# Optimization experiments

Measured on AMD Instinct MI355X. Metric: run time of the kernel, lower is better.

The kernel has to match this reference:

```python
import jax, jax.numpy as jnp
import numpy as np

N, DIM, TOPK = 8192, 512, 10


def setup_inputs() -> dict:
    key = jax.random.key(0)
    k1, k2, k3, k4, k5 = jax.random.split(key, 5)
    s = DIM ** -0.5
    return {
        "X": jax.random.normal(k1, (N, DIM), dtype=jnp.float32),
        "Wh": jax.random.normal(k2, (DIM, DIM), dtype=jnp.float32) * s,
        "bh": jax.random.normal(k3, (DIM,), dtype=jnp.float32) * s,
        "Wt": jax.random.normal(k4, (DIM, DIM), dtype=jnp.float32) * s,
        "bt": jax.random.normal(k5, (DIM,), dtype=jnp.float32) * s,
    }


def reference(X, Wh, bh, Wt, bt):
    n, dim = X.shape
    scale = dim ** -0.5
    e_h = X @ Wh.T + bh                      # [n, dim]
    e_t = X @ Wt.T + bt                      # [n, dim]
    logits = (e_h @ e_t.T) * scale           # [n, n]
    topk_val, topk_idx = jax.lax.top_k(logits, TOPK)   # [n, k]
    weights = jax.nn.softmax(topk_val, axis=-1)        # [n, k]
    src = jnp.repeat(jnp.arange(n, dtype=jnp.int32), TOPK)  # [n*k]
    dst = topk_idx.reshape(-1).astype(jnp.int32)
    edge_index = jnp.stack([src, dst], axis=0)          # [2, n*k]
    edge_weight = weights.reshape(-1)                   # [n*k]
    return edge_index, edge_weight
```

## Files before the change

### kernel.cpp

```cpp
#include <hip/hip_runtime.h>
#include <math.h>

#define NROWS 8192
#define DIMK  512
#define TOPK  10
#define SCALE 0.044194173824159223f

#define ETM 128
#define ETN 64
#define ETK 32
#define NTHREADS 256

#define BM 128
#define BN 128
#define BK 32
#define NS2 16
#define SCOLS2 (NROWS / NS2)
#define NQ 256
#define CAP 64
#define TMARGIN 2.0f

typedef __attribute__((ext_vector_type(8))) short bf16x8;
typedef __attribute__((ext_vector_type(4))) float f32x4;

__device__ __forceinline__ unsigned short f2bf(float f) {
  unsigned int u = __float_as_uint(f);
  u = (u + 0x7FFF + ((u >> 16) & 1)) >> 16;
  return (unsigned short)u;
}

__device__ __forceinline__ void gld16(const void* g, const void* lds) {
  __builtin_amdgcn_global_load_lds(
      (const __attribute__((address_space(1))) void*)g,
      (__attribute__((address_space(3))) void*)lds, 16, 0, 0);
}

__global__ __launch_bounds__(NTHREADS, 4)
void embed_gemm(const float* __restrict__ X,
                const float* __restrict__ Wh, const float* __restrict__ bh,
                const float* __restrict__ Wt, const float* __restrict__ bt,
                float* __restrict__ Eh, float* __restrict__ Et,
                unsigned short* __restrict__ Ehb, unsigned short* __restrict__ Etb) {
  __shared__ float As[ETK][ETM + 4];
  __shared__ float Bs[ETK][ETN + 4];

  const int tid = threadIdx.x;
  const int rowBase = blockIdx.x * ETM;
  const int colBase = blockIdx.y * ETN;
  const float* W  = (colBase < DIMK) ? Wh : Wt;
  const float* bb = (colBase < DIMK) ? bh : bt;
  float* Out            = (colBase < DIMK) ? Eh : Et;
  unsigned short* Outb  = (colBase < DIMK) ? Ehb : Etb;
  const int colOff = colBase & (DIMK - 1);

  const int tx = tid & 15, ty = tid >> 4;
  float acc[8][4];
#pragma unroll
  for (int r = 0; r < 8; ++r)
#pragma unroll
    for (int c = 0; c < 4; ++c) acc[r][c] = 0.f;

  for (int kt = 0; kt < DIMK; kt += ETK) {
    __syncthreads();
#pragma unroll
    for (int u = 0; u < 4; ++u) {
      const int idx = tid + u * NTHREADS;
      const int r = idx >> 3;
      const int dc = idx & 7;
      const float4 av = *(const float4*)&X[(size_t)(rowBase + r) * DIMK + kt + dc * 4];
      As[dc * 4 + 0][r] = av.x; As[dc * 4 + 1][r] = av.y;
      As[dc * 4 + 2][r] = av.z; As[dc * 4 + 3][r] = av.w;
    }
#pragma unroll
    for (int u = 0; u < 2; ++u) {
      const int idx = tid + u * NTHREADS;
      const int r = idx >> 3;
      const int dc = idx & 7;
      const float4 bv = *(const float4*)&W[(size_t)(colOff + r) * DIMK + kt + dc * 4];
      Bs[dc * 4 + 0][r] = bv.x; Bs[dc * 4 + 1][r] = bv.y;
      Bs[dc * 4 + 2][r] = bv.z; Bs[dc * 4 + 3][r] = bv.w;
    }
    __syncthreads();
#pragma unroll 8
    for (int k = 0; k < ETK; ++k) {
      const float4 a0 = *(const float4*)&As[k][ty * 4];
      const float4 a1 = *(const float4*)&As[k][64 + ty * 4];
      const float4 b  = *(const float4*)&Bs[k][tx * 4];
      const float ar[8] = {a0.x, a0.y, a0.z, a0.w, a1.x, a1.y, a1.z, a1.w};
      const float br[4] = {b.x, b.y, b.z, b.w};
#pragma unroll
      for (int r = 0; r < 8; ++r)
#pragma unroll
        for (int c = 0; c < 4; ++c)
          acc[r][c] = fmaf(ar[r], br[c], acc[r][c]);
    }
  }

  const float4 bv = *(const float4*)&bb[colOff + tx * 4];
  const float br[4] = {bv.x, bv.y, bv.z, bv.w};
#pragma unroll
  for (int r = 0; r < 8; ++r) {
    const int row = rowBase + ((r < 4) ? (ty * 4 + r) : (64 + ty * 4 + r - 4));
    float4 o;
    o.x = acc[r][0] + br[0]; o.y = acc[r][1] + br[1];
    o.z = acc[r][2] + br[2]; o.w = acc[r][3] + br[3];
    const size_t off = (size_t)row * DIMK + colOff + tx * 4;
    *(float4*)&Out[off] = o;
    ushort4 ob;
    ob.x = f2bf(o.x); ob.y = f2bf(o.y); ob.z = f2bf(o.z); ob.w = f2bf(o.w);
    *(ushort4*)&Outb[off] = ob;
  }
}

__global__ __launch_bounds__(256, 3)
void screen_store(const unsigned short* __restrict__ Ehb,
                  const unsigned short* __restrict__ Etb,
                  float* __restrict__ tmax, unsigned short* __restrict__ Sc) {
  __shared__ unsigned short As[2][BM * BK];
  __shared__ unsigned short Bs[2][BN * BK];
  __shared__ unsigned short Csb[BM * 72];

  const int tid = threadIdx.x;
  const int rowBase = blockIdx.x * BM;
  const int strip = blockIdx.y;
  const int w = tid >> 6, lane = tid & 63;
  const int q = lane >> 4, l15 = lane & 15;
  const int wr = (w & 1) * 64, wc = (w >> 1) * 64;
  const int rr = tid >> 1, hq = tid & 1;

  const int c0 = tid, c1 = tid + 256;
  const int wb0 = __builtin_amdgcn_readfirstlane(tid & ~63);
  const int wb1 = wb0 + 256;
  const int ar0 = c0 >> 2, ac0 = (c0 & 3) * 8;
  const int ar1 = c1 >> 2, ac1 = (c1 & 3) * 8;

  for (int ct = 0; ct < SCOLS2; ct += BN) {
    const int colBase = strip * SCOLS2 + ct;
    const int tileG = colBase >> 7;
    f32x4 acc[4][4];
#pragma unroll
    for (int i = 0; i < 4; ++i)
#pragma unroll
      for (int j = 0; j < 4; ++j) acc[i][j] = (f32x4){0.f, 0.f, 0.f, 0.f};

    auto stage = [&](int buf, int kt) {
      gld16(Ehb + (size_t)(rowBase + ar0) * DIMK + kt + ac0, As[buf] + wb0 * 8);
      gld16(Ehb + (size_t)(rowBase + ar1) * DIMK + kt + ac1, As[buf] + wb1 * 8);
      gld16(Etb + (size_t)(colBase + ar0) * DIMK + kt + ac0, Bs[buf] + wb0 * 8);
      gld16(Etb + (size_t)(colBase + ar1) * DIMK + kt + ac1, Bs[buf] + wb1 * 8);
    };
    auto compute = [&](int buf) {
      bf16x8 af[4], bf[4];
#pragma unroll
      for (int i = 0; i < 4; ++i)
        af[i] = *(const bf16x8*)&As[buf][(wr + i * 16 + l15) * BK + q * 8];
#pragma unroll
      for (int j = 0; j < 4; ++j)
        bf[j] = *(const bf16x8*)&Bs[buf][(wc + j * 16 + l15) * BK + q * 8];
#pragma unroll
      for (int i = 0; i < 4; ++i)
#pragma unroll
        for (int j = 0; j < 4; ++j)
          acc[i][j] = __builtin_amdgcn_mfma_f32_16x16x32_bf16(af[i], bf[j], acc[i][j], 0, 0, 0);
    };

    stage(0, 0);
    __syncthreads();
#pragma unroll 1
    for (int ki = 0; ki < DIMK / BK; ki += 2) {
      if (ki + 1 < DIMK / BK) stage(1, (ki + 1) * BK);
      compute(0);
      __syncthreads();
      if (ki + 2 < DIMK / BK) stage(0, (ki + 2) * BK);
      compute(1);
      __syncthreads();
    }

#pragma unroll
    for (int half = 0; half < 2; ++half) {
      if ((w >> 1) == half) {
#pragma unroll
        for (int i = 0; i < 4; ++i)
#pragma unroll
          for (int j = 0; j < 4; ++j)
#pragma unroll
            for (int rg = 0; rg < 4; ++rg)
              Csb[(wr + i * 16 + q * 4 + rg) * 72 + j * 16 + l15] = f2bf(acc[i][j][rg]);
      }
      __syncthreads();
      float m = -INFINITY;
      uint4 buf4[4];
#pragma unroll
      for (int k = 0; k < 4; ++k) {
        buf4[k] = *(const uint4*)&Csb[rr * 72 + hq * 32 + k * 8];
        const unsigned int uu[4] = {buf4[k].x, buf4[k].y, buf4[k].z, buf4[k].w};
#pragma unroll
        for (int e = 0; e < 4; ++e) {
          m = fmaxf(m, __uint_as_float(uu[e] << 16));
          m = fmaxf(m, __uint_as_float(uu[e] & 0xFFFF0000u));
        }
      }
      tmax[(size_t)(rowBase + rr) * NQ + tileG * 4 + half * 2 + hq] = m;
      uint4* dst = (uint4*)&Sc[(size_t)(rowBase + rr) * NROWS + colBase + half * 64 + hq * 32];
#pragma unroll
      for (int k = 0; k < 4; ++k) dst[k] = buf4[k];
      __syncthreads();
    }
  }
}

__global__ __launch_bounds__(256)
void collect_scan(const unsigned short* __restrict__ Sc,
                  const float* __restrict__ tmax,
                  int* __restrict__ cnt, int* __restrict__ cand) {
  __shared__ int lcnt[4];
  const int lane = threadIdx.x & 63;
  const int wid = threadIdx.x >> 6;
  const int r = blockIdx.x * 4 + wid;

  if (threadIdx.x < 4) lcnt[threadIdx.x] = 0;
  __syncthreads();

  const f32x4 gm = *(const f32x4*)&tmax[(size_t)r * NQ + lane * 4];
  float a0 = gm[0], a1 = gm[1], a2 = gm[2], a3 = gm[3];
  float g = -INFINITY;
#pragma unroll 1
  for (int j = 0; j < TOPK; ++j) {
    const float lm = fmaxf(fmaxf(a0, a1), fmaxf(a2, a3));
    g = lm;
#pragma unroll
    for (int off = 32; off > 0; off >>= 1) g = fmaxf(g, __shfl_xor(g, off, 64));
    const unsigned long long ball = __ballot(lm == g);
    const int src = __ffsll((long long)ball) - 1;
    if (lane == src) {
      if      (a0 == g) a0 = -INFINITY;
      else if (a1 == g) a1 = -INFINITY;
      else if (a2 == g) a2 = -INFINITY;
      else              a3 = -INFINITY;
    }
  }
  const float tt = g - TMARGIN;

  const unsigned short* row = Sc + (size_t)r * NROWS;
#pragma unroll 1
  for (int it = 0; it < NROWS / 512; ++it) {
    const int c0 = it * 512 + lane * 8;
    const uint4 u = *(const uint4*)&row[c0];
    const unsigned int uu[4] = {u.x, u.y, u.z, u.w};
#pragma unroll
    for (int e = 0; e < 4; ++e) {
      const float lo = __uint_as_float(uu[e] << 16);
      const float hi = __uint_as_float(uu[e] & 0xFFFF0000u);
      if (lo >= tt) {
        const int p = atomicAdd(&lcnt[wid], 1);
        if (p < CAP) cand[(size_t)r * CAP + p] = c0 + 2 * e;
      }
      if (hi >= tt) {
        const int p = atomicAdd(&lcnt[wid], 1);
        if (p < CAP) cand[(size_t)r * CAP + p] = c0 + 2 * e + 1;
      }
    }
  }
  __syncthreads();
  if (threadIdx.x < 4) cnt[blockIdx.x * 4 + threadIdx.x] = min(lcnt[threadIdx.x], CAP);
}

__global__ __launch_bounds__(256)
void rescore_topk(const float* __restrict__ Eh, const float* __restrict__ Et,
                  const int* __restrict__ cnt, const int* __restrict__ cand,
                  float* __restrict__ out) {
  const int lane = threadIdx.x & 63;
  const int r = blockIdx.x * 4 + (threadIdx.x >> 6);
  const int n = cnt[r];
  const bool active = lane < n;
  const int col = active ? cand[(size_t)r * CAP + lane] : 0;

  const float* a = Eh + (size_t)r * DIMK;
  const float* b = Et + (size_t)col * DIMK;
  float p = 0.f;
#pragma unroll 4
  for (int k = 0; k < DIMK; k += 4) {
    const float4 av = *(const float4*)&a[k];
    const float4 bv = *(const float4*)&b[k];
    p = fmaf(av.x, bv.x, p);
    p = fmaf(av.y, bv.y, p);
    p = fmaf(av.z, bv.z, p);
    p = fmaf(av.w, bv.w, p);
  }
  float v = active ? p * SCALE : -INFINITY;
  const int vc = active ? col : 0x7FFFFFFF;

  float myv = -INFINITY; int myc = 0; float m = 0.f;
  float vv = v; int cc2 = vc;
#pragma unroll 1
  for (int j = 0; j < TOPK; ++j) {
    float bvv = vv; int bcc = cc2;
#pragma unroll
    for (int off = 32; off > 0; off >>= 1) {
      const float ov = __shfl_xor(bvv, off, 64);
      const int oc = __shfl_xor(bcc, off, 64);
      if (ov > bvv || (ov == bvv && oc < bcc)) { bvv = ov; bcc = oc; }
    }
    if (j == 0) m = bvv;
    if (lane == j) { myv = bvv; myc = bcc; }
    if (vv == bvv && cc2 == bcc) vv = -INFINITY;
  }

  float sum = 0.f;
#pragma unroll
  for (int j = 0; j < TOPK; ++j) sum += expf(__shfl(myv, j, 64) - m);
  const float inv = 1.0f / sum;

  if (lane < TOPK) {
    const size_t ro = (size_t)r * TOPK + lane;
    out[ro] = (float)r;
    out[(size_t)NROWS * TOPK + ro] = (float)myc;
    out[2 * (size_t)NROWS * TOPK + ro] = expf(myv - m) * inv;
  }
}

extern "C" void kernel_launch(void* const* d_in, const int* in_sizes, int n_in,
                              void* d_out, int out_size, void* d_ws, size_t ws_size,
                              hipStream_t stream) {
  const float* X  = (const float*)d_in[0];
  const float* Wh = (const float*)d_in[1];
  const float* bh = (const float*)d_in[2];
  const float* Wt = (const float*)d_in[3];
  const float* bt = (const float*)d_in[4];
  float* out = (float*)d_out;

  char* ws = (char*)d_ws;
  const size_t embB  = (size_t)NROWS * DIMK * sizeof(float);
  const size_t embBH = (size_t)NROWS * DIMK * sizeof(unsigned short);
  const size_t tmaxB = (size_t)NROWS * NQ * sizeof(float);
  const size_t cntB  = (size_t)NROWS * sizeof(int);
  const size_t candB = (size_t)NROWS * CAP * sizeof(int);
  float* Eh   = (float*)ws;
  float* Et   = (float*)(ws + embB);
  unsigned short* Ehb = (unsigned short*)(ws + 2 * embB);
  unsigned short* Etb = (unsigned short*)(ws + 2 * embB + embBH);
  float* tmax = (float*)(ws + 2 * embB + 2 * embBH);
  int*   cnt  = (int*)(ws + 2 * embB + 2 * embBH + tmaxB);
  int*   cand = (int*)(ws + 2 * embB + 2 * embBH + tmaxB + cntB);
  unsigned short* Sc = (unsigned short*)
      (ws + 2 * embB + 2 * embBH + tmaxB + cntB + candB);

  dim3 blk(NTHREADS);
  dim3 g1(NROWS / ETM, (2 * DIMK) / ETN);
  embed_gemm<<<g1, blk, 0, stream>>>(X, Wh, bh, Wt, bt, Eh, Et, Ehb, Etb);

  dim3 g2(NROWS / BM, NS2);
  screen_store<<<g2, blk, 0, stream>>>(Ehb, Etb, tmax, Sc);

  collect_scan<<<NROWS / 4, blk, 0, stream>>>(Sc, tmax, cnt, cand);

  rescore_topk<<<NROWS / 4, blk, 0, stream>>>(Eh, Et, cnt, cand, out);
}
```

Measured before the change: 429.4 us.

## Double-buffer embed GEMM LDS tiles and fuse candidate scan with rescore

The embedding GEMM now stages K-tiles into two LDS buffers so the next tile's global loads overlap the current tile's FMAs. This halves the barriers per tile but raises LDS use, and the occupancy hint drops to 3. The collect and rescore kernels are merged, so candidates stay in shared memory instead of round-tripping through global cnt/cand arrays, which also removes one kernel launch. The fused kernel holds more state per block, which may affect occupancy.

```diff
diff --git a/kernel.cpp b/kernel.cpp
--- a/kernel.cpp
+++ b/kernel.cpp
@@ -35,14 +35,14 @@
       (__attribute__((address_space(3))) void*)lds, 16, 0, 0);
 }
 
-__global__ __launch_bounds__(NTHREADS, 4)
+__global__ __launch_bounds__(NTHREADS, 3)
 void embed_gemm(const float* __restrict__ X,
                 const float* __restrict__ Wh, const float* __restrict__ bh,
                 const float* __restrict__ Wt, const float* __restrict__ bt,
                 float* __restrict__ Eh, float* __restrict__ Et,
                 unsigned short* __restrict__ Ehb, unsigned short* __restrict__ Etb) {
-  __shared__ float As[ETK][ETM + 4];
-  __shared__ float Bs[ETK][ETN + 4];
+  __shared__ float As[2][ETK][ETM + 4];
+  __shared__ float Bs[2][ETK][ETN + 4];
 
   const int tid = threadIdx.x;
   const int rowBase = blockIdx.x * ETM;
@@ -60,16 +60,15 @@
 #pragma unroll
     for (int c = 0; c < 4; ++c) acc[r][c] = 0.f;
 
-  for (int kt = 0; kt < DIMK; kt += ETK) {
-    __syncthreads();
+  auto stage = [&](int buf, int kt) {
 #pragma unroll
     for (int u = 0; u < 4; ++u) {
       const int idx = tid + u * NTHREADS;
       const int r = idx >> 3;
       const int dc = idx & 7;
       const float4 av = *(const float4*)&X[(size_t)(rowBase + r) * DIMK + kt + dc * 4];
-      As[dc * 4 + 0][r] = av.x; As[dc * 4 + 1][r] = av.y;
-      As[dc * 4 + 2][r] = av.z; As[dc * 4 + 3][r] = av.w;
+      As[buf][dc * 4 + 0][r] = av.x; As[buf][dc * 4 + 1][r] = av.y;
+      As[buf][dc * 4 + 2][r] = av.z; As[buf][dc * 4 + 3][r] = av.w;
     }
 #pragma unroll
     for (int u = 0; u < 2; ++u) {
@@ -77,15 +76,16 @@
       const int r = idx >> 3;
       const int dc = idx & 7;
       const float4 bv = *(const float4*)&W[(size_t)(colOff + r) * DIMK + kt + dc * 4];
-      Bs[dc * 4 + 0][r] = bv.x; Bs[dc * 4 + 1][r] = bv.y;
-      Bs[dc * 4 + 2][r] = bv.z; Bs[dc * 4 + 3][r] = bv.w;
-    }
-    __syncthreads();
-#pragma unroll 8
+      Bs[buf][dc * 4 + 0][r] = bv.x; Bs[buf][dc * 4 + 1][r] = bv.y;
+      Bs[buf][dc * 4 + 2][r] = bv.z; Bs[buf][dc * 4 + 3][r] = bv.w;
+    }
+  };
+  auto compute = [&](int buf) {
+#pragma unroll 4
     for (int k = 0; k < ETK; ++k) {
-      const float4 a0 = *(const float4*)&As[k][ty * 4];
-      const float4 a1 = *(const float4*)&As[k][64 + ty * 4];
-      const float4 b  = *(const float4*)&Bs[k][tx * 4];
+      const float4 a0 = *(const float4*)&As[buf][k][ty * 4];
+      const float4 a1 = *(const float4*)&As[buf][k][64 + ty * 4];
+      const float4 b  = *(const float4*)&Bs[buf][k][tx * 4];
       const float ar[8] = {a0.x, a0.y, a0.z, a0.w, a1.x, a1.y, a1.z, a1.w};
       const float br[4] = {b.x, b.y, b.z, b.w};
 #pragma unroll
@@ -94,6 +94,18 @@
         for (int c = 0; c < 4; ++c)
           acc[r][c] = fmaf(ar[r], br[c], acc[r][c]);
     }
+  };
+
+  stage(0, 0);
+  __syncthreads();
+#pragma unroll 1
+  for (int ki = 0; ki < DIMK / ETK; ki += 2) {
+    if (ki + 1 < DIMK / ETK) stage(1, (ki + 1) * ETK);
+    compute(0);
+    __syncthreads();
+    if (ki + 2 < DIMK / ETK) stage(0, (ki + 2) * ETK);
+    compute(1);
+    __syncthreads();
   }
 
   const float4 bv = *(const float4*)&bb[colOff + tx * 4];
@@ -210,15 +222,17 @@
 }
 
 __global__ __launch_bounds__(256)
-void collect_scan(const unsigned short* __restrict__ Sc,
-                  const float* __restrict__ tmax,
-                  int* __restrict__ cnt, int* __restrict__ cand) {
+void collect_rescore(const unsigned short* __restrict__ Sc,
+                     const float* __restrict__ tmax,
+                     const float* __restrict__ Eh, const float* __restrict__ Et,
+                     float* __restrict__ out) {
   __shared__ int lcnt[4];
+  __shared__ int lcand[4][CAP];
   const int lane = threadIdx.x & 63;
   const int wid = threadIdx.x >> 6;
   const int r = blockIdx.x * 4 + wid;
 
-  if (threadIdx.x < 4) lcnt[threadIdx.x] = 0;
+  if (lane == 0) lcnt[wid] = 0;
   __syncthreads();
 
   const f32x4 gm = *(const f32x4*)&tmax[(size_t)r * NQ + lane * 4];
@@ -244,8 +258,8 @@
   const unsigned short* row = Sc + (size_t)r * NROWS;
 #pragma unroll 1
   for (int it = 0; it < NROWS / 512; ++it) {
-    const int c0 = it * 512 + lane * 8;
-    const uint4 u = *(const uint4*)&row[c0];
+    const int cc0 = it * 512 + lane * 8;
+    const uint4 u = *(const uint4*)&row[cc0];
     const unsigned int uu[4] = {u.x, u.y, u.z, u.w};
 #pragma unroll
     for (int e = 0; e < 4; ++e) {
@@ -253,27 +267,19 @@
       const float hi = __uint_as_float(uu[e] & 0xFFFF0000u);
       if (lo >= tt) {
         const int p = atomicAdd(&lcnt[wid], 1);
-        if (p < CAP) cand[(size_t)r * CAP + p] = c0 + 2 * e;
+        if (p < CAP) lcand[wid][p] = cc0 + 2 * e;
       }
       if (hi >= tt) {
         const int p = atomicAdd(&lcnt[wid], 1);
-        if (p < CAP) cand[(size_t)r * CAP + p] = c0 + 2 * e + 1;
+        if (p < CAP) lcand[wid][p] = cc0 + 2 * e + 1;
       }
     }
   }
   __syncthreads();
-  if (threadIdx.x < 4) cnt[blockIdx.x * 4 + threadIdx.x] = min(lcnt[threadIdx.x], CAP);
-}
-
-__global__ __launch_bounds__(256)
-void rescore_topk(const float* __restrict__ Eh, const float* __restrict__ Et,
-                  const int* __restrict__ cnt, const int* __restrict__ cand,
-                  float* __restrict__ out) {
-  const int lane = threadIdx.x & 63;
-  const int r = blockIdx.x * 4 + (threadIdx.x >> 6);
-  const int n = cnt[r];
+
+  const int n = min(lcnt[wid], CAP);
   const bool active = lane < n;
-  const int col = active ? cand[(size_t)r * CAP + lane] : 0;
+  const int col = active ? lcand[wid][lane] : 0;
 
   const float* a = Eh + (size_t)r * DIMK;
   const float* b = Et + (size_t)col * DIMK;
@@ -333,17 +339,12 @@
   const size_t embB  = (size_t)NROWS * DIMK * sizeof(float);
   const size_t embBH = (size_t)NROWS * DIMK * sizeof(unsigned short);
   const size_t tmaxB = (size_t)NROWS * NQ * sizeof(float);
-  const size_t cntB  = (size_t)NROWS * sizeof(int);
-  const size_t candB = (size_t)NROWS * CAP * sizeof(int);
   float* Eh   = (float*)ws;
   float* Et   = (float*)(ws + embB);
   unsigned short* Ehb = (unsigned short*)(ws + 2 * embB);
   unsigned short* Etb = (unsigned short*)(ws + 2 * embB + embBH);
   float* tmax = (float*)(ws + 2 * embB + 2 * embBH);
-  int*   cnt  = (int*)(ws + 2 * embB + 2 * embBH + tmaxB);
-  int*   cand = (int*)(ws + 2 * embB + 2 * embBH + tmaxB + cntB);
-  unsigned short* Sc = (unsigned short*)
-      (ws + 2 * embB + 2 * embBH + tmaxB + cntB + candB);
+  unsigned short* Sc = (unsigned short*)(ws + 2 * embB + 2 * embBH + tmaxB);
 
   dim3 blk(NTHREADS);
   dim3 g1(NROWS / ETM, (2 * DIMK) / ETN);
@@ -352,7 +353,5 @@
   dim3 g2(NROWS / BM, NS2);
   screen_store<<<g2, blk, 0, stream>>>(Ehb, Etb, tmax, Sc);
 
-  collect_scan<<<NROWS / 4, blk, 0, stream>>>(Sc, tmax, cnt, cand);
-
-  rescore_topk<<<NROWS / 4, blk, 0, stream>>>(Eh, Et, cnt, cand, out);
-}
+  collect_rescore<<<NROWS / 4, blk, 0, stream>>>(Sc, tmax, Eh, Et, out);
+}
```

Result: faster. 417.5 us (-2.8%).
